# Kernel optimization log

Measured on AMD Instinct MI355X. Metric: run time of the kernel, lower is better.

Reference implementation:

```python
import jax, jax.numpy as jnp
import numpy as np

COMMITMENT_COST = 0.25
NUM_CODES = 4096
EMBED_DIM = 64


def setup_inputs() -> dict:
    key = jax.random.key(0)
    k1, k2 = jax.random.split(key)
    z_e = jax.random.normal(k1, (65536, EMBED_DIM), dtype=jnp.float32)
    embeddings = jax.random.normal(k2, (NUM_CODES, EMBED_DIM), dtype=jnp.float32)
    return {"z_e": z_e, "embeddings": embeddings}


def reference(z_e, embeddings):
    # Squared Euclidean distances; argmin is identical to torch.cdist argmin.
    # d2[n,k] = |z_e[n]|^2 - 2 z_e[n].e[k] + |e[k]|^2
    z_sq = jnp.sum(z_e * z_e, axis=-1, keepdims=True)            # [N,1]
    e_sq = jnp.sum(embeddings * embeddings, axis=-1)              # [K]
    d2 = z_sq - 2.0 * jnp.einsum('nd,kd->nk', z_e, embeddings) + e_sq  # [N,K]
    indices = jnp.argmin(d2, axis=-1)                             # [N] int
    z_q = embeddings[indices]                                     # [N,D] gather

    # commitment loss = mse(stop_grad(z_q), z_e)
    commitment_loss = COMMITMENT_COST * jnp.mean(
        (jax.lax.stop_gradient(z_q) - z_e) ** 2)

    # straight-through estimator
    z_q_st = z_e + jax.lax.stop_gradient(z_q - z_e)

    # code usage stats: one-hot mean == normalized histogram (scatter-add)
    n = z_e.shape[0]
    counts = jnp.zeros((NUM_CODES,), dtype=jnp.float32).at[indices].add(1.0)
    avg_probs = counts / n
    perplexity = jnp.exp(-jnp.sum(avg_probs * jnp.log(avg_probs + 1e-10)))
    n_active = jnp.sum(avg_probs > 0.001)

    return z_q_st, indices, commitment_loss, perplexity, n_active
```

## Files before the change

### kernel.cpp

```cpp
#include <hip/hip_runtime.h>
#include <math.h>

#define D 64
#define K 4096
#define MARGIN 0.015f
#define KSPLIT 4
#define CPH (K / 16 / KSPLIT)

typedef float f32x4 __attribute__((ext_vector_type(4)));
typedef short bf16x8 __attribute__((ext_vector_type(8)));

static __device__ inline unsigned short f2bf(float x) {
  unsigned u = __builtin_bit_cast(unsigned, x);
  unsigned r = (u + 0x7FFF + ((u >> 16) & 1)) >> 16;
  return (unsigned short)r;
}
static __device__ inline float bf2f(unsigned short s) {
  unsigned u = ((unsigned)s) << 16;
  return __builtin_bit_cast(float, u);
}

__global__ __launch_bounds__(256) void esq_kernel(const float* __restrict__ emb,
                                                  float* __restrict__ e_sq) {
  int k = blockIdx.x * 256 + threadIdx.x;
  if (k >= K) return;
  const float* e = emb + (size_t)k * D;
  float s = 0.f;
#pragma unroll
  for (int d = 0; d < D; ++d) s = fmaf(e[d], e[d], s);
  e_sq[k] = s;
}

__global__ __launch_bounds__(256) void esplit_kernel(const float* __restrict__ emb,
                                                     short* __restrict__ e_hi,
                                                     short* __restrict__ e_lo) {
  int i = blockIdx.x * 256 + threadIdx.x;
  if (i >= (K / 16) * 2 * 64) return;
  int lane = i & 63;
  int t = (i >> 6) & 1;
  int c = i >> 7;
  int quad = lane >> 4, col = lane & 15;
  const float* src = emb + (size_t)(c * 16 + col) * D + t * 32 + quad * 8;
  f32x4 u0 = *(const f32x4*)src;
  f32x4 u1 = *(const f32x4*)(src + 4);
  bf16x8 h, l;
#pragma unroll
  for (int j = 0; j < 8; ++j) {
    float x = (j < 4) ? u0[j] : u1[j - 4];
    unsigned short hb = f2bf(x);
    h[j] = (short)hb;
    l[j] = (short)f2bf(x - bf2f(hb));
  }
  size_t dst = ((size_t)i) * 8;
  *(bf16x8*)(e_hi + dst) = h;
  *(bf16x8*)(e_lo + dst) = l;
}

__global__ __launch_bounds__(256, 2) void dist_kernel(const float* __restrict__ z_e,
                                                      const short* __restrict__ e_hi,
                                                      const short* __restrict__ e_lo,
                                                      const float* __restrict__ esq,
                                                      float* __restrict__ pbest,
                                                      float* __restrict__ psec,
                                                      int* __restrict__ pidx) {
  const int tid = threadIdx.x;
  const int wv = tid >> 6;
  const int lane = tid & 63;
  const int quad = lane >> 4, col = lane & 15;
  const int rowbase = blockIdx.x * 128 + wv * 32;
  const int half = blockIdx.y;
  const int c0 = half * CPH;

  bf16x8 a_hi[2][2], a_lo[2][2];
#pragma unroll
  for (int s = 0; s < 2; ++s) {
#pragma unroll
    for (int t = 0; t < 2; ++t) {
      const float* zr = z_e + (size_t)(rowbase + s * 16 + col) * D + t * 32 + quad * 8;
      f32x4 u0 = *(const f32x4*)zr;
      f32x4 u1 = *(const f32x4*)(zr + 4);
#pragma unroll
      for (int j = 0; j < 8; ++j) {
        float x = (j < 4) ? u0[j] : u1[j - 4];
        unsigned short hb = f2bf(x);
        a_hi[s][t][j] = (short)hb;
        a_lo[s][t][j] = (short)f2bf(x - bf2f(hb));
      }
    }
  }

  float best[8], second[8];
  int bidx[8];
#pragma unroll
  for (int i = 0; i < 8; ++i) {
    best[i] = __builtin_inff();
    second[i] = __builtin_inff();
    bidx[i] = 0;
  }

  const size_t lofs = (size_t)lane * 8;

  for (int cc = 0; cc < CPH; ++cc) {
    const int c = c0 + cc;
    const bf16x8 bh0 = *(const bf16x8*)(e_hi + (size_t)(c * 2 + 0) * 512 + lofs);
    const bf16x8 bh1 = *(const bf16x8*)(e_hi + (size_t)(c * 2 + 1) * 512 + lofs);
    const bf16x8 bl0 = *(const bf16x8*)(e_lo + (size_t)(c * 2 + 0) * 512 + lofs);
    const bf16x8 bl1 = *(const bf16x8*)(e_lo + (size_t)(c * 2 + 1) * 512 + lofs);
    const float esql = esq[c * 16 + col];
    const int code = c * 16 + col;

    f32x4 acc0 = {0.f, 0.f, 0.f, 0.f};
    f32x4 acc1 = {0.f, 0.f, 0.f, 0.f};
    acc0 = __builtin_amdgcn_mfma_f32_16x16x32_bf16(a_hi[0][0], bh0, acc0, 0, 0, 0);
    acc1 = __builtin_amdgcn_mfma_f32_16x16x32_bf16(a_hi[1][0], bh0, acc1, 0, 0, 0);
    acc0 = __builtin_amdgcn_mfma_f32_16x16x32_bf16(a_lo[0][0], bh0, acc0, 0, 0, 0);
    acc1 = __builtin_amdgcn_mfma_f32_16x16x32_bf16(a_lo[1][0], bh0, acc1, 0, 0, 0);
    acc0 = __builtin_amdgcn_mfma_f32_16x16x32_bf16(a_hi[0][0], bl0, acc0, 0, 0, 0);
    acc1 = __builtin_amdgcn_mfma_f32_16x16x32_bf16(a_hi[1][0], bl0, acc1, 0, 0, 0);
    acc0 = __builtin_amdgcn_mfma_f32_16x16x32_bf16(a_hi[0][1], bh1, acc0, 0, 0, 0);
    acc1 = __builtin_amdgcn_mfma_f32_16x16x32_bf16(a_hi[1][1], bh1, acc1, 0, 0, 0);
    acc0 = __builtin_amdgcn_mfma_f32_16x16x32_bf16(a_lo[0][1], bh1, acc0, 0, 0, 0);
    acc1 = __builtin_amdgcn_mfma_f32_16x16x32_bf16(a_lo[1][1], bh1, acc1, 0, 0, 0);
    acc0 = __builtin_amdgcn_mfma_f32_16x16x32_bf16(a_hi[0][1], bl1, acc0, 0, 0, 0);
    acc1 = __builtin_amdgcn_mfma_f32_16x16x32_bf16(a_hi[1][1], bl1, acc1, 0, 0, 0);

#pragma unroll
    for (int r = 0; r < 4; ++r) {
      float q = fmaf(-2.f, acc0[r], esql);
      float ob = best[r];
      best[r] = fminf(ob, q);
      second[r] = __builtin_amdgcn_fmed3f(ob, q, second[r]);
      bidx[r] = (q < ob) ? code : bidx[r];
    }
#pragma unroll
    for (int r = 0; r < 4; ++r) {
      float q = fmaf(-2.f, acc1[r], esql);
      float ob = best[4 + r];
      best[4 + r] = fminf(ob, q);
      second[4 + r] = __builtin_amdgcn_fmed3f(ob, q, second[4 + r]);
      bidx[4 + r] = (q < ob) ? code : bidx[4 + r];
    }
  }

#pragma unroll
  for (int i = 0; i < 8; ++i) {
    float b = best[i], s2 = second[i];
    int ix = bidx[i];
#pragma unroll
    for (int off = 1; off < 16; off <<= 1) {
      float ob = __shfl_xor(b, off);
      float os = __shfl_xor(s2, off);
      int oi = __shfl_xor(ix, off);
      float ns = fminf(fminf(s2, os), fmaxf(b, ob));
      if (ob < b || (ob == b && oi < ix)) ix = oi;
      b = fminf(b, ob);
      s2 = ns;
    }
    if (col == 0) {
      int row = rowbase + (i >> 2) * 16 + quad * 4 + (i & 3);
      size_t o = (size_t)half * 65536 + row;
      pbest[o] = b;
      psec[o] = s2;
      pidx[o] = ix;
    }
  }
}

__global__ __launch_bounds__(256) void merge_kernel(const float* __restrict__ pbest,
                                                    const float* __restrict__ psec,
                                                    const int* __restrict__ pidx,
                                                    int* __restrict__ best_idx,
                                                    int* __restrict__ worklist,
                                                    int* __restrict__ nwork,
                                                    int N) {
  int row = blockIdx.x * 256 + threadIdx.x;
  float b = pbest[row];
  float s2 = psec[row];
  int ix = pidx[row];
#pragma unroll
  for (int h = 1; h < KSPLIT; ++h) {
    size_t o = (size_t)h * 65536 + row;
    float bh = pbest[o];
    float sh = psec[o];
    int ih = pidx[o];
    s2 = fminf(fminf(s2, sh), fmaxf(b, bh));
    if (bh < b) ix = ih;
    b = fminf(b, bh);
  }
  best_idx[row] = ix;
  if (s2 - b < MARGIN) {
    int slot = atomicAdd(nwork, 1);
    worklist[slot] = row;
  }
}

__global__ __launch_bounds__(256, 1) void resolve_kernel(const float* __restrict__ z_e,
                                                         const float* __restrict__ emb,
                                                         const float* __restrict__ esq,
                                                         const float* __restrict__ pbest,
                                                         const float* __restrict__ psec,
                                                         const int* __restrict__ pidx,
                                                         const int* __restrict__ worklist,
                                                         const int* __restrict__ nwork,
                                                         int* __restrict__ best_idx) {
  const int tid = threadIdx.x;
  const int wave = tid >> 6;
  const int lane = tid & 63;
  const int wgid = blockIdx.x * 4 + wave;

  __shared__ float zs[4][D];
  const int n = *nwork;

  for (int j = wgid; j < n; j += 1024) {
    const int row = worklist[j];
    if (lane < 16) ((f32x4*)zs[wave])[lane] = *((const f32x4*)(z_e + (size_t)row * D) + lane);

    float pb[KSPLIT], ps[KSPLIT];
    int pi[KSPLIT];
    float B = __builtin_inff();
#pragma unroll
    for (int h = 0; h < KSPLIT; ++h) {
      size_t o = (size_t)h * 65536 + row;
      pb[h] = pbest[o];
      ps[h] = psec[o];
      pi[h] = pidx[o];
      B = fminf(B, pb[h]);
    }
    const float lim = B + MARGIN;

    float bv = __builtin_inff();
    int bi = 0;
#pragma unroll
    for (int h = 0; h < KSPLIT; ++h) {
      if (ps[h] < lim) {
        float hb = __builtin_inff();
        int hx = 0;
        for (int t = 0; t < 16; ++t) {
          int c = h * 1024 + t * 64 + lane;
          const f32x4* er = (const f32x4*)(emb + (size_t)c * D);
          f32x4 a = {0.f, 0.f, 0.f, 0.f};
#pragma unroll
          for (int i = 0; i < 16; ++i)
            a = __builtin_elementwise_fma(er[i], ((const f32x4*)zs[wave])[i], a);
          float dot = (a[0] + a[1]) + (a[2] + a[3]);
          float q = fmaf(-2.f, dot, esq[c]);
          if (q < hb) { hb = q; hx = c; }
        }
#pragma unroll
        for (int off = 32; off > 0; off >>= 1) {
          float ov = __shfl_down(hb, off);
          int oi = __shfl_down(hx, off);
          if (ov < hb || (ov == hb && oi < hx)) { hb = ov; hx = oi; }
        }
        hb = __shfl(hb, 0);
        hx = __shfl(hx, 0);
        if (hb < bv || (hb == bv && hx < bi)) { bv = hb; bi = hx; }
      } else if (pb[h] < lim) {
        int c = pi[h];
        float p = emb[(size_t)c * D + lane] * zs[wave][lane];
#pragma unroll
        for (int off = 1; off < 64; off <<= 1) p += __shfl_xor(p, off);
        float q = fmaf(-2.f, p, esq[c]);
        if (q < bv || (q == bv && c < bi)) { bv = q; bi = c; }
      }
    }
    if (lane == 0) best_idx[row] = bi;
  }
}

__global__ __launch_bounds__(256) void finalize_kernel(const float* __restrict__ z_e,
                                                       const float* __restrict__ emb,
                                                       const int* __restrict__ best_idx,
                                                       float* __restrict__ out_zq,
                                                       float* __restrict__ out_idx,
                                                       int* __restrict__ counts,
                                                       float* __restrict__ block_loss) {
  const int tid = threadIdx.x;
  const int wave = tid >> 6;
  const int lane = tid & 63;
  const int row = blockIdx.x * 4 + wave;

  int bidx = best_idx[row];
  float ze = z_e[(size_t)row * D + lane];
  float zq = emb[(size_t)bidx * D + lane];
  float st = ze + (zq - ze);
  out_zq[(size_t)row * D + lane] = st;

  float diff = zq - ze;
  float sq = diff * diff;
#pragma unroll
  for (int off = 32; off > 0; off >>= 1) sq += __shfl_down(sq, off);

  __shared__ float ls[4];
  if (lane == 0) {
    ls[wave] = sq;
    out_idx[row] = (float)bidx;
    atomicAdd(&counts[bidx], 1);
  }
  __syncthreads();
  if (tid == 0) block_loss[blockIdx.x] = ls[0] + ls[1] + ls[2] + ls[3];
}

__global__ __launch_bounds__(1024) void stats_kernel(const float* __restrict__ block_loss,
                                                     int nblocks,
                                                     const int* __restrict__ counts,
                                                     float* __restrict__ out_scalars,
                                                     int N) {
  const int tid = threadIdx.x;
  const int wave = tid >> 6;
  const int lane = tid & 63;

  float lsum = 0.f;
  for (int i = tid; i < nblocks; i += 1024) lsum += block_loss[i];

  float ent = 0.f;
  int act = 0;
  const float invN = 1.0f / (float)N;
  for (int k = tid; k < K; k += 1024) {
    float p = (float)counts[k] * invN;
    ent += p * logf(p + 1e-10f);
    act += (p > 0.001f) ? 1 : 0;
  }

#pragma unroll
  for (int off = 32; off > 0; off >>= 1) {
    lsum += __shfl_down(lsum, off);
    ent += __shfl_down(ent, off);
    act += __shfl_down(act, off);
  }

  __shared__ float sl[16], se[16];
  __shared__ int sa[16];
  if (lane == 0) { sl[wave] = lsum; se[wave] = ent; sa[wave] = act; }
  __syncthreads();
  if (tid == 0) {
    float L = 0.f, E = 0.f;
    int A = 0;
#pragma unroll
    for (int w = 0; w < 16; ++w) { L += sl[w]; E += se[w]; A += sa[w]; }
    out_scalars[0] = 0.25f * L / ((float)N * (float)D);
    out_scalars[1] = expf(-E);
    out_scalars[2] = (float)A;
  }
}

extern "C" void kernel_launch(void* const* d_in, const int* in_sizes, int n_in,
                              void* d_out, int out_size, void* d_ws, size_t ws_size,
                              hipStream_t stream) {
  const float* z_e = (const float*)d_in[0];
  const float* emb = (const float*)d_in[1];
  const int N = in_sizes[0] / D;

  float* out = (float*)d_out;
  float* out_zq = out;
  float* out_idx = out + (size_t)N * D;
  float* out_scalars = out + (size_t)N * (D + 1);

  char* ws = (char*)d_ws;
  size_t o = 0;
  int* counts = (int*)(ws + o);      o += 16384;
  int* nwork = (int*)(ws + o);       o += 256;
  float* esq = (float*)(ws + o);     o += 16384;
  short* e_hi = (short*)(ws + o);    o += (size_t)K * D * 2;
  short* e_lo = (short*)(ws + o);    o += (size_t)K * D * 2;
  float* pbest = (float*)(ws + o);   o += (size_t)KSPLIT * N * 4;
  float* psec = (float*)(ws + o);    o += (size_t)KSPLIT * N * 4;
  int* pidx = (int*)(ws + o);        o += (size_t)KSPLIT * N * 4;
  int* best_idx = (int*)(ws + o);    o += (size_t)N * 4;
  int* worklist = (int*)(ws + o);    o += (size_t)N * 4;
  float* block_loss = (float*)(ws + o);

  hipMemsetAsync(counts, 0, 16384 + 256, stream);

  esq_kernel<<<K / 256, 256, 0, stream>>>(emb, esq);
  esplit_kernel<<<(K / 16) * 2 * 64 / 256, 256, 0, stream>>>(emb, e_hi, e_lo);
  dist_kernel<<<dim3(N / 128, KSPLIT), 256, 0, stream>>>(z_e, e_hi, e_lo, esq,
                                                         pbest, psec, pidx);
  merge_kernel<<<N / 256, 256, 0, stream>>>(pbest, psec, pidx, best_idx,
                                            worklist, nwork, N);
  resolve_kernel<<<256, 256, 0, stream>>>(z_e, emb, esq, pbest, psec, pidx,
                                          worklist, nwork, best_idx);
  finalize_kernel<<<N / 4, 256, 0, stream>>>(z_e, emb, best_idx, out_zq, out_idx,
                                             counts, block_loss);
  stats_kernel<<<1, 1024, 0, stream>>>(block_loss, N / 4, counts, out_scalars, N);
}
```

Before: 248.8 us.

## Use fp16 embeddings with split-z MFMA, seeded accumulators and prefetched codebook

The codebook is now stored as a single fp16 copy instead of bf16 hi/lo halves. Only z_e is split into hi/lo fp16, which cuts the MFMA count per chunk from 12 to 8 and halves the codebook traffic. The accumulator is seeded with -0.5*|e|^2 so the per-element fma disappears, the argmin becomes a max (rescaled by -2 at the end), and the next chunk's codebook loads are software-prefetched. Because fp16 rounding of the codebook is less exact, the resolve margin is widened and resolve gets twice as many blocks, which may send more rows through the exact fallback path.

```diff
diff --git a/kernel.cpp b/kernel.cpp
--- a/kernel.cpp
+++ b/kernel.cpp
@@ -3,22 +3,12 @@
 
 #define D 64
 #define K 4096
-#define MARGIN 0.015f
+#define MARGIN 0.08f
 #define KSPLIT 4
 #define CPH (K / 16 / KSPLIT)
 
 typedef float f32x4 __attribute__((ext_vector_type(4)));
-typedef short bf16x8 __attribute__((ext_vector_type(8)));
-
-static __device__ inline unsigned short f2bf(float x) {
-  unsigned u = __builtin_bit_cast(unsigned, x);
-  unsigned r = (u + 0x7FFF + ((u >> 16) & 1)) >> 16;
-  return (unsigned short)r;
-}
-static __device__ inline float bf2f(unsigned short s) {
-  unsigned u = ((unsigned)s) << 16;
-  return __builtin_bit_cast(float, u);
-}
+typedef _Float16 f16x8 __attribute__((ext_vector_type(8)));
 
 __global__ __launch_bounds__(256) void esq_kernel(const float* __restrict__ emb,
                                                   float* __restrict__ e_sq) {
@@ -32,8 +22,7 @@
 }
 
 __global__ __launch_bounds__(256) void esplit_kernel(const float* __restrict__ emb,
-                                                     short* __restrict__ e_hi,
-                                                     short* __restrict__ e_lo) {
+                                                     short* __restrict__ e_h) {
   int i = blockIdx.x * 256 + threadIdx.x;
   if (i >= (K / 16) * 2 * 64) return;
   int lane = i & 63;
@@ -43,22 +32,17 @@
   const float* src = emb + (size_t)(c * 16 + col) * D + t * 32 + quad * 8;
   f32x4 u0 = *(const f32x4*)src;
   f32x4 u1 = *(const f32x4*)(src + 4);
-  bf16x8 h, l;
+  f16x8 h;
 #pragma unroll
   for (int j = 0; j < 8; ++j) {
     float x = (j < 4) ? u0[j] : u1[j - 4];
-    unsigned short hb = f2bf(x);
-    h[j] = (short)hb;
-    l[j] = (short)f2bf(x - bf2f(hb));
-  }
-  size_t dst = ((size_t)i) * 8;
-  *(bf16x8*)(e_hi + dst) = h;
-  *(bf16x8*)(e_lo + dst) = l;
+    h[j] = (_Float16)x;
+  }
+  *(f16x8*)(e_h + (size_t)i * 8) = h;
 }
 
 __global__ __launch_bounds__(256, 2) void dist_kernel(const float* __restrict__ z_e,
-                                                      const short* __restrict__ e_hi,
-                                                      const short* __restrict__ e_lo,
+                                                      const short* __restrict__ e_h,
                                                       const float* __restrict__ esq,
                                                       float* __restrict__ pbest,
                                                       float* __restrict__ psec,
@@ -71,7 +55,7 @@
   const int half = blockIdx.y;
   const int c0 = half * CPH;
 
-  bf16x8 a_hi[2][2], a_lo[2][2];
+  f16x8 a_hi[2][2], a_lo[2][2];
 #pragma unroll
   for (int s = 0; s < 2; ++s) {
 #pragma unroll
@@ -82,9 +66,9 @@
 #pragma unroll
       for (int j = 0; j < 8; ++j) {
         float x = (j < 4) ? u0[j] : u1[j - 4];
-        unsigned short hb = f2bf(x);
-        a_hi[s][t][j] = (short)hb;
-        a_lo[s][t][j] = (short)f2bf(x - bf2f(hb));
+        _Float16 h = (_Float16)x;
+        a_hi[s][t][j] = h;
+        a_lo[s][t][j] = (_Float16)(x - (float)h);
       }
     }
   }
@@ -93,58 +77,64 @@
   int bidx[8];
 #pragma unroll
   for (int i = 0; i < 8; ++i) {
-    best[i] = __builtin_inff();
-    second[i] = __builtin_inff();
+    best[i] = -__builtin_inff();
+    second[i] = -__builtin_inff();
     bidx[i] = 0;
   }
 
-  const size_t lofs = (size_t)lane * 8;
+  const short* pB = e_h + (size_t)c0 * 1024 + (size_t)lane * 8;
+  const float* pE = esq + c0 * 16 + col;
+  f16x8 b0 = *(const f16x8*)pB;
+  f16x8 b1 = *(const f16x8*)(pB + 512);
+  float eq = *pE;
+  int code = c0 * 16 + col;
 
   for (int cc = 0; cc < CPH; ++cc) {
-    const int c = c0 + cc;
-    const bf16x8 bh0 = *(const bf16x8*)(e_hi + (size_t)(c * 2 + 0) * 512 + lofs);
-    const bf16x8 bh1 = *(const bf16x8*)(e_hi + (size_t)(c * 2 + 1) * 512 + lofs);
-    const bf16x8 bl0 = *(const bf16x8*)(e_lo + (size_t)(c * 2 + 0) * 512 + lofs);
-    const bf16x8 bl1 = *(const bf16x8*)(e_lo + (size_t)(c * 2 + 1) * 512 + lofs);
-    const float esql = esq[c * 16 + col];
-    const int code = c * 16 + col;
-
-    f32x4 acc0 = {0.f, 0.f, 0.f, 0.f};
-    f32x4 acc1 = {0.f, 0.f, 0.f, 0.f};
-    acc0 = __builtin_amdgcn_mfma_f32_16x16x32_bf16(a_hi[0][0], bh0, acc0, 0, 0, 0);
-    acc1 = __builtin_amdgcn_mfma_f32_16x16x32_bf16(a_hi[1][0], bh0, acc1, 0, 0, 0);
-    acc0 = __builtin_amdgcn_mfma_f32_16x16x32_bf16(a_lo[0][0], bh0, acc0, 0, 0, 0);
-    acc1 = __builtin_amdgcn_mfma_f32_16x16x32_bf16(a_lo[1][0], bh0, acc1, 0, 0, 0);
-    acc0 = __builtin_amdgcn_mfma_f32_16x16x32_bf16(a_hi[0][0], bl0, acc0, 0, 0, 0);
-    acc1 = __builtin_amdgcn_mfma_f32_16x16x32_bf16(a_hi[1][0], bl0, acc1, 0, 0, 0);
-    acc0 = __builtin_amdgcn_mfma_f32_16x16x32_bf16(a_hi[0][1], bh1, acc0, 0, 0, 0);
-    acc1 = __builtin_amdgcn_mfma_f32_16x16x32_bf16(a_hi[1][1], bh1, acc1, 0, 0, 0);
-    acc0 = __builtin_amdgcn_mfma_f32_16x16x32_bf16(a_lo[0][1], bh1, acc0, 0, 0, 0);
-    acc1 = __builtin_amdgcn_mfma_f32_16x16x32_bf16(a_lo[1][1], bh1, acc1, 0, 0, 0);
-    acc0 = __builtin_amdgcn_mfma_f32_16x16x32_bf16(a_hi[0][1], bl1, acc0, 0, 0, 0);
-    acc1 = __builtin_amdgcn_mfma_f32_16x16x32_bf16(a_hi[1][1], bl1, acc1, 0, 0, 0);
+    pB += 1024;
+    pE += 16;
+    f16x8 n0 = *(const f16x8*)pB;
+    f16x8 n1 = *(const f16x8*)(pB + 512);
+    float neq = *pE;
+
+    const float seed = -0.5f * eq;
+    f32x4 acc0 = {seed, seed, seed, seed};
+    f32x4 acc1 = acc0;
+    acc0 = __builtin_amdgcn_mfma_f32_16x16x32_f16(a_hi[0][0], b0, acc0, 0, 0, 0);
+    acc1 = __builtin_amdgcn_mfma_f32_16x16x32_f16(a_hi[1][0], b0, acc1, 0, 0, 0);
+    acc0 = __builtin_amdgcn_mfma_f32_16x16x32_f16(a_lo[0][0], b0, acc0, 0, 0, 0);
+    acc1 = __builtin_amdgcn_mfma_f32_16x16x32_f16(a_lo[1][0], b0, acc1, 0, 0, 0);
+    acc0 = __builtin_amdgcn_mfma_f32_16x16x32_f16(a_hi[0][1], b1, acc0, 0, 0, 0);
+    acc1 = __builtin_amdgcn_mfma_f32_16x16x32_f16(a_hi[1][1], b1, acc1, 0, 0, 0);
+    acc0 = __builtin_amdgcn_mfma_f32_16x16x32_f16(a_lo[0][1], b1, acc0, 0, 0, 0);
+    acc1 = __builtin_amdgcn_mfma_f32_16x16x32_f16(a_lo[1][1], b1, acc1, 0, 0, 0);
 
 #pragma unroll
     for (int r = 0; r < 4; ++r) {
-      float q = fmaf(-2.f, acc0[r], esql);
+      float q = acc0[r];
       float ob = best[r];
-      best[r] = fminf(ob, q);
+      best[r] = fmaxf(ob, q);
       second[r] = __builtin_amdgcn_fmed3f(ob, q, second[r]);
-      bidx[r] = (q < ob) ? code : bidx[r];
+      bidx[r] = (q > ob) ? code : bidx[r];
     }
 #pragma unroll
     for (int r = 0; r < 4; ++r) {
-      float q = fmaf(-2.f, acc1[r], esql);
+      float q = acc1[r];
       float ob = best[4 + r];
-      best[4 + r] = fminf(ob, q);
+      best[4 + r] = fmaxf(ob, q);
       second[4 + r] = __builtin_amdgcn_fmed3f(ob, q, second[4 + r]);
-      bidx[4 + r] = (q < ob) ? code : bidx[4 + r];
-    }
+      bidx[4 + r] = (q > ob) ? code : bidx[4 + r];
+    }
+
+    b0 = n0;
+    b1 = n1;
+    eq = neq;
+    code += 16;
   }
 
 #pragma unroll
   for (int i = 0; i < 8; ++i) {
-    float b = best[i], s2 = second[i];
+    float b = -2.f * best[i];
+    float s2 = -2.f * second[i];
     int ix = bidx[i];
 #pragma unroll
     for (int off = 1; off < 16; off <<= 1) {
@@ -207,11 +197,12 @@
   const int wave = tid >> 6;
   const int lane = tid & 63;
   const int wgid = blockIdx.x * 4 + wave;
+  const int wstep = gridDim.x * 4;
 
   __shared__ float zs[4][D];
   const int n = *nwork;
 
-  for (int j = wgid; j < n; j += 1024) {
+  for (int j = wgid; j < n; j += wstep) {
     const int row = worklist[j];
     if (lane < 16) ((f32x4*)zs[wave])[lane] = *((const f32x4*)(z_e + (size_t)row * D) + lane);
 
@@ -361,8 +352,8 @@
   int* counts = (int*)(ws + o);      o += 16384;
   int* nwork = (int*)(ws + o);       o += 256;
   float* esq = (float*)(ws + o);     o += 16384;
-  short* e_hi = (short*)(ws + o);    o += (size_t)K * D * 2;
-  short* e_lo = (short*)(ws + o);    o += (size_t)K * D * 2;
+  short* e_h = (short*)(ws + o);     o += (size_t)K * D * 2;
+  o += 4096;
   float* pbest = (float*)(ws + o);   o += (size_t)KSPLIT * N * 4;
   float* psec = (float*)(ws + o);    o += (size_t)KSPLIT * N * 4;
   int* pidx = (int*)(ws + o);        o += (size_t)KSPLIT * N * 4;
@@ -373,12 +364,12 @@
   hipMemsetAsync(counts, 0, 16384 + 256, stream);
 
   esq_kernel<<<K / 256, 256, 0, stream>>>(emb, esq);
-  esplit_kernel<<<(K / 16) * 2 * 64 / 256, 256, 0, stream>>>(emb, e_hi, e_lo);
-  dist_kernel<<<dim3(N / 128, KSPLIT), 256, 0, stream>>>(z_e, e_hi, e_lo, esq,
+  esplit_kernel<<<(K / 16) * 2 * 64 / 256, 256, 0, stream>>>(emb, e_h);
+  dist_kernel<<<dim3(N / 128, KSPLIT), 256, 0, stream>>>(z_e, e_h, esq,
                                                          pbest, psec, pidx);
   merge_kernel<<<N / 256, 256, 0, stream>>>(pbest, psec, pidx, best_idx,
                                             worklist, nwork, N);
-  resolve_kernel<<<256, 256, 0, stream>>>(z_e, emb, esq, pbest, psec, pidx,
+  resolve_kernel<<<512, 256, 0, stream>>>(z_e, emb, esq, pbest, psec, pidx,
                                           worklist, nwork, best_idx);
   finalize_kernel<<<N / 4, 256, 0, stream>>>(z_e, emb, best_idx, out_zq, out_idx,
                                              counts, block_loss);
```

Result: faster. 230.3 us (-7.4%).
